# Performance work log

Measured on AMD Instinct MI355X. Metric: run time of the kernel, lower is better.

## Reference

```python
import jax, jax.numpy as jnp
import numpy as np

N, D, H, E, K = 8192, 1024, 4096, 8, 2


def setup_inputs() -> dict:
    key = jax.random.key(0)
    ks = jax.random.split(key, 4)
    scaled = lambda k, shp, fan: (jax.random.normal(k, shp, jnp.float32) / np.sqrt(fan).astype(np.float32))
    return {
        "x": jax.random.normal(ks[0], (N, D), jnp.float32),
        "Wg": scaled(ks[1], (D, E), D),
        "bg": jnp.zeros((E,), jnp.float32),
        "W1": scaled(ks[2], (E, D, H), D),
        "b1": jnp.zeros((E, H), jnp.float32),
        "W2": scaled(ks[3], (E, H, D), H),
        "b2": jnp.zeros((E, D), jnp.float32),
    }


def reference(x, Wg, bg, W1, b1, W2, b2):
    # Gating: softmax over experts, top-k selection, renormalize top-k probs.
    gate_probs = jax.nn.softmax(x @ Wg + bg, axis=-1)            # [N, E]
    topk_p, topk_i = jax.lax.top_k(gate_probs, K)                # [N, K]
    topk_p = topk_p / topk_p.sum(axis=-1, keepdims=True)
    onehot = jax.nn.one_hot(topk_i, E, dtype=x.dtype)            # [N, K, E]
    # Per-token combine weight for each expert (0 if expert not in top-k).
    w = (onehot * topk_p[..., None]).sum(axis=1)                 # [N, E]

    out = jnp.zeros_like(x)
    for e in range(E):  # fixed small loop over structurally distinct experts
        h = jax.nn.relu(x @ W1[e] + b1[e])                       # dropout = identity (eval)
        out = out + w[:, e:e + 1] * (h @ W2[e] + b2[e])

    # Load-balancing auxiliary loss.
    importance = gate_probs.sum(axis=0)
    importance = importance / importance.sum()
    load = onehot.sum(axis=(0, 1)) / (x.shape[0] * K)            # [E]
    lb_loss = E * (importance * load).sum()
    return out, lb_loss
```

## Files before the change

### kernel.cpp

```cpp
#include <hip/hip_runtime.h>
#include <hip/hip_bf16.h>
#include <math.h>

#define NTOK 8192
#define DDIM 1024
#define HDIM 4096
#define NEXP 8
#define KTOP 2
#define MAXROWS 17408
#define MAXTILES 136

typedef __bf16 bf16x8 __attribute__((ext_vector_type(8)));
typedef float f32x4 __attribute__((ext_vector_type(4)));

#define GAS __attribute__((address_space(1)))
#define LAS __attribute__((address_space(3)))

__device__ __forceinline__ void async16(const void* g, void* l) {
  __builtin_amdgcn_global_load_lds((GAS void*)g, (LAS void*)l, 16, 0, 0);
}

#define XB_OFF     ((size_t)0)
#define W1T_OFF    (XB_OFF + (size_t)NTOK*DDIM*2)
#define W2T_OFF    (W1T_OFF + (size_t)NEXP*DDIM*HDIM*2)
#define HB_OFF     (W2T_OFF + (size_t)NEXP*HDIM*DDIM*2)
#define ROWTOK_OFF (HB_OFF + (size_t)MAXROWS*HDIM*2)
#define ROWW_OFF   (ROWTOK_OFF + (size_t)MAXROWS*4)
#define TOKE_OFF   (ROWW_OFF + (size_t)MAXROWS*4)
#define TOKW_OFF   (TOKE_OFF + (size_t)NTOK*KTOP*4)
#define TILEE_OFF  (TOKW_OFF + (size_t)NTOK*KTOP*4)
#define CNT_OFF    (TILEE_OFF + (size_t)256*4)
#define POS_OFF    (CNT_OFF + 64)
#define IMP_OFF    (POS_OFF + 64)
#define META_OFF   (IMP_OFF + 64)

__global__ void init_kernel(int* counts, float* importance) {
  if (threadIdx.x < NEXP) { counts[threadIdx.x] = 0; importance[threadIdx.x] = 0.f; }
}

__global__ void zero_out_kernel(float* __restrict__ out) {
  size_t i = ((size_t)blockIdx.x * blockDim.x + threadIdx.x) * 4;
  if (i < (size_t)NTOK * DDIM) {
    *(float4*)(out + i) = make_float4(0.f, 0.f, 0.f, 0.f);
  }
}

__global__ void cast_x_kernel(const float* __restrict__ src, __hip_bfloat16* __restrict__ dst) {
  size_t i = ((size_t)blockIdx.x * blockDim.x + threadIdx.x) * 4;
  if (i < (size_t)NTOK * DDIM) {
    float4 v = *(const float4*)(src + i);
    dst[i + 0] = __float2bfloat16(v.x);
    dst[i + 1] = __float2bfloat16(v.y);
    dst[i + 2] = __float2bfloat16(v.z);
    dst[i + 3] = __float2bfloat16(v.w);
  }
}

__global__ __launch_bounds__(256) void transpose_cast_kernel(
    const float* __restrict__ src, __hip_bfloat16* __restrict__ dst, int R, int C) {
  __shared__ float tile[64][65];
  const int e = blockIdx.z;
  const float* s = src + (size_t)e * R * C;
  __hip_bfloat16* d = dst + (size_t)e * R * C;
  const int c0 = blockIdx.x * 64, r0 = blockIdx.y * 64;
  const int tx = threadIdx.x & 63, ty = threadIdx.x >> 6;
#pragma unroll
  for (int i = ty; i < 64; i += 4)
    tile[i][tx] = s[(size_t)(r0 + i) * C + c0 + tx];
  __syncthreads();
#pragma unroll
  for (int i = ty; i < 64; i += 4)
    d[(size_t)(c0 + i) * R + r0 + tx] = __float2bfloat16(tile[tx][i]);
}

__global__ __launch_bounds__(256) void gating_kernel(
    const float* __restrict__ x, const float* __restrict__ Wg, const float* __restrict__ bg,
    int* __restrict__ tok_e, float* __restrict__ tok_w,
    int* __restrict__ counts, float* __restrict__ importance) {
  const int tid = threadIdx.x, wid = tid >> 6, lane = tid & 63;
  const int t = blockIdx.x * 32 + wid * 8 + (lane >> 3);
  const int e = lane & 7;
  const float* xr = x + (size_t)t * DDIM;
  double dot = 0.0;
  for (int d = 0; d < DDIM; d += 4) {
    float4 xv = *(const float4*)(xr + d);
    dot += (double)xv.x * (double)Wg[(d + 0) * NEXP + e];
    dot += (double)xv.y * (double)Wg[(d + 1) * NEXP + e];
    dot += (double)xv.z * (double)Wg[(d + 2) * NEXP + e];
    dot += (double)xv.w * (double)Wg[(d + 3) * NEXP + e];
  }
  double logit = dot + (double)bg[e];
  double m = logit;
  for (int off = 1; off < 8; off <<= 1) {
    double o = __shfl_xor(m, off, 64);
    m = o > m ? o : m;
  }
  double p = exp(logit - m);
  double s = p;
  for (int off = 1; off < 8; off <<= 1) s += __shfl_xor(s, off, 64);
  float prob = (float)(p / s);

  __shared__ float imp[NEXP];
  __shared__ int cnt[NEXP];
  if (tid < NEXP) { imp[tid] = 0.f; cnt[tid] = 0; }
  __syncthreads();
  atomicAdd(&imp[e], prob);

  float bp = prob; int be = e;
  for (int off = 1; off < 8; off <<= 1) {
    float op = __shfl_xor(bp, off, 64); int oe = __shfl_xor(be, off, 64);
    if (op > bp || (op == bp && oe < be)) { bp = op; be = oe; }
  }
  float p2 = (e == be) ? -1.f : prob;
  float sp = p2; int se = e;
  for (int off = 1; off < 8; off <<= 1) {
    float op = __shfl_xor(sp, off, 64); int oe = __shfl_xor(se, off, 64);
    if (op > sp || (op == sp && oe < se)) { sp = op; se = oe; }
  }
  if (e == 0) {
    float tsum = bp + sp;
    tok_e[t * 2 + 0] = be; tok_e[t * 2 + 1] = se;
    tok_w[t * 2 + 0] = bp / tsum; tok_w[t * 2 + 1] = sp / tsum;
    atomicAdd(&cnt[be], 1); atomicAdd(&cnt[se], 1);
  }
  __syncthreads();
  if (tid < NEXP) {
    atomicAdd(&counts[tid], cnt[tid]);
    atomicAdd(&importance[tid], imp[tid]);
  }
}

__global__ void offsets_kernel(const int* __restrict__ counts, int* pos, int* tile_expert,
                               int* meta, int* row_token) {
  if (threadIdx.x == 0) {
    int pb = 0, tb = 0;
    for (int e = 0; e < NEXP; e++) {
      pos[e] = pb;
      int tiles = (counts[e] + 127) >> 7;
      for (int tt = 0; tt < tiles; ++tt) tile_expert[tb + tt] = e;
      pb += tiles * 128; tb += tiles;
    }
    meta[0] = tb;
  }
  __syncthreads();
  for (int i = threadIdx.x; i < MAXROWS; i += blockDim.x) row_token[i] = -1;
}

__global__ void scatter_kernel(const int* __restrict__ tok_e, const float* __restrict__ tok_w,
                               int* __restrict__ pos, int* __restrict__ row_token,
                               float* __restrict__ row_weight) {
  __shared__ int lcnt[NEXP], lbase[NEXP];
  const int t = blockIdx.x * 256 + threadIdx.x;
  if (threadIdx.x < NEXP) lcnt[threadIdx.x] = 0;
  __syncthreads();
  const int e0 = tok_e[t * 2 + 0], e1 = tok_e[t * 2 + 1];
  const int s0 = atomicAdd(&lcnt[e0], 1);
  const int s1 = atomicAdd(&lcnt[e1], 1);
  __syncthreads();
  if (threadIdx.x < NEXP) lbase[threadIdx.x] = atomicAdd(&pos[threadIdx.x], lcnt[threadIdx.x]);
  __syncthreads();
  int r0 = lbase[e0] + s0; row_token[r0] = t; row_weight[r0] = tok_w[t * 2 + 0];
  int r1 = lbase[e1] + s1; row_token[r1] = t; row_weight[r1] = tok_w[t * 2 + 1];
}

__global__ __launch_bounds__(256) void gemm1_kernel(
    const __hip_bfloat16* __restrict__ xb, const __hip_bfloat16* __restrict__ w1t,
    const float* __restrict__ b1, __hip_bfloat16* __restrict__ hb,
    const int* __restrict__ row_token, const int* __restrict__ tile_expert,
    const int* __restrict__ meta) {
  const int tile_y = blockIdx.y;
  if (tile_y >= meta[0]) return;
  const int n0 = blockIdx.x * 128;
  const int e = tile_expert[tile_y];
  const int r0 = tile_y * 128;
  const int tid = threadIdx.x;
  const int wid = tid >> 6, lane = tid & 63;

  __shared__ __align__(16) __hip_bfloat16 As[128 * 32];
  __shared__ __align__(16) __hip_bfloat16 Bs[128 * 32];

  const int srow = wid * 32 + (lane >> 2);
  const int scol = (lane & 3) * 8;
  int t0 = row_token[r0 + srow];      if (t0 < 0) t0 = 0;
  int t1 = row_token[r0 + srow + 16]; if (t1 < 0) t1 = 0;
  const __hip_bfloat16* ga0 = xb + (size_t)t0 * DDIM + scol;
  const __hip_bfloat16* ga1 = xb + (size_t)t1 * DDIM + scol;
  const __hip_bfloat16* gb0 = w1t + ((size_t)e * HDIM + n0 + srow) * DDIM + scol;
  const __hip_bfloat16* gb1 = gb0 + (size_t)16 * DDIM;
  __hip_bfloat16* lA0 = &As[(wid * 32 + 0) * 32];
  __hip_bfloat16* lA1 = &As[(wid * 32 + 16) * 32];
  __hip_bfloat16* lB0 = &Bs[(wid * 32 + 0) * 32];
  __hip_bfloat16* lB1 = &Bs[(wid * 32 + 16) * 32];

  f32x4 acc[4][4] = {};
  const int wm = (wid & 1) * 64, wn = (wid >> 1) * 64;
  const int fr = lane & 15;
  const int kq = (lane >> 4) * 8;

  for (int kt = 0; kt < DDIM / 32; ++kt) {
    __syncthreads();
    async16(ga0, lA0); async16(ga1, lA1);
    async16(gb0, lB0); async16(gb1, lB1);
    ga0 += 32; ga1 += 32; gb0 += 32; gb1 += 32;
    __syncthreads();
    bf16x8 av[4], bv[4];
#pragma unroll
    for (int i = 0; i < 4; i++) av[i] = *(const bf16x8*)&As[(wm + i * 16 + fr) * 32 + kq];
#pragma unroll
    for (int j = 0; j < 4; j++) bv[j] = *(const bf16x8*)&Bs[(wn + j * 16 + fr) * 32 + kq];
#pragma unroll
    for (int i = 0; i < 4; i++)
#pragma unroll
      for (int j = 0; j < 4; j++)
        acc[i][j] = __builtin_amdgcn_mfma_f32_16x16x32_bf16(av[i], bv[j], acc[i][j], 0, 0, 0);
  }

  const int crow = (lane >> 4) * 4;
  const int ccol = lane & 15;
#pragma unroll
  for (int j = 0; j < 4; j++) {
    const int gc = n0 + wn + j * 16 + ccol;
    const float bias = b1[e * HDIM + gc];
#pragma unroll
    for (int i = 0; i < 4; i++) {
      const int grb = r0 + wm + i * 16 + crow;
#pragma unroll
      for (int r = 0; r < 4; r++) {
        float v = acc[i][j][r] + bias;
        v = v > 0.f ? v : 0.f;
        hb[(size_t)(grb + r) * HDIM + gc] = __float2bfloat16(v);
      }
    }
  }
}

__global__ __launch_bounds__(256) void gemm2_kernel(
    const __hip_bfloat16* __restrict__ hb, const __hip_bfloat16* __restrict__ w2t,
    const float* __restrict__ b2, float* __restrict__ out,
    const int* __restrict__ row_token, const float* __restrict__ row_weight,
    const int* __restrict__ tile_expert, const int* __restrict__ meta) {
  const int tile_y = blockIdx.y;
  if (tile_y >= meta[0]) return;
  const int n0 = blockIdx.x * 128;
  const int e = tile_expert[tile_y];
  const int r0 = tile_y * 128;
  const int tid = threadIdx.x;
  const int wid = tid >> 6, lane = tid & 63;

  __shared__ __align__(16) __hip_bfloat16 As[128 * 32];
  __shared__ __align__(16) __hip_bfloat16 Bs[128 * 32];

  const int srow = wid * 32 + (lane >> 2);
  const int scol = (lane & 3) * 8;
  const __hip_bfloat16* ga0 = hb + (size_t)(r0 + srow) * HDIM + scol;
  const __hip_bfloat16* ga1 = ga0 + (size_t)16 * HDIM;
  const __hip_bfloat16* gb0 = w2t + ((size_t)e * DDIM + n0 + srow) * HDIM + scol;
  const __hip_bfloat16* gb1 = gb0 + (size_t)16 * HDIM;
  __hip_bfloat16* lA0 = &As[(wid * 32 + 0) * 32];
  __hip_bfloat16* lA1 = &As[(wid * 32 + 16) * 32];
  __hip_bfloat16* lB0 = &Bs[(wid * 32 + 0) * 32];
  __hip_bfloat16* lB1 = &Bs[(wid * 32 + 16) * 32];

  f32x4 acc[4][4] = {};
  const int wm = (wid & 1) * 64, wn = (wid >> 1) * 64;
  const int fr = lane & 15;
  const int kq = (lane >> 4) * 8;

  for (int kt = 0; kt < HDIM / 32; ++kt) {
    __syncthreads();
    async16(ga0, lA0); async16(ga1, lA1);
    async16(gb0, lB0); async16(gb1, lB1);
    ga0 += 32; ga1 += 32; gb0 += 32; gb1 += 32;
    __syncthreads();
    bf16x8 av[4], bv[4];
#pragma unroll
    for (int i = 0; i < 4; i++) av[i] = *(const bf16x8*)&As[(wm + i * 16 + fr) * 32 + kq];
#pragma unroll
    for (int j = 0; j < 4; j++) bv[j] = *(const bf16x8*)&Bs[(wn + j * 16 + fr) * 32 + kq];
#pragma unroll
    for (int i = 0; i < 4; i++)
#pragma unroll
      for (int j = 0; j < 4; j++)
        acc[i][j] = __builtin_amdgcn_mfma_f32_16x16x32_bf16(av[i], bv[j], acc[i][j], 0, 0, 0);
  }

  const int crow = (lane >> 4) * 4;
  const int ccol = lane & 15;
#pragma unroll
  for (int i = 0; i < 4; i++) {
#pragma unroll
    for (int r = 0; r < 4; r++) {
      const int rr = r0 + wm + i * 16 + crow + r;
      const int tok = row_token[rr];
      if (tok < 0) continue;
      const float w = row_weight[rr];
#pragma unroll
      for (int j = 0; j < 4; j++) {
        const int gc = n0 + wn + j * 16 + ccol;
        float v = w * (acc[i][j][r] + b2[e * DDIM + gc]);
        atomicAdd(out + (size_t)tok * DDIM + gc, v);
      }
    }
  }
}

__global__ void finalize_kernel(const float* __restrict__ importance,
                                const int* __restrict__ counts, float* __restrict__ lb_out) {
  if (threadIdx.x == 0 && blockIdx.x == 0) {
    float s = 0.f;
    for (int e = 0; e < NEXP; e++) s += importance[e];
    float lb = 0.f;
    for (int e = 0; e < NEXP; e++)
      lb += (importance[e] / s) * ((float)counts[e] / (float)(NTOK * KTOP));
    lb_out[0] = (float)NEXP * lb;
  }
}

extern "C" void kernel_launch(void* const* d_in, const int* in_sizes, int n_in,
                              void* d_out, int out_size, void* d_ws, size_t ws_size,
                              hipStream_t stream) {
  (void)in_sizes; (void)n_in; (void)out_size; (void)ws_size;
  const float* x  = (const float*)d_in[0];
  const float* Wg = (const float*)d_in[1];
  const float* bg = (const float*)d_in[2];
  const float* W1 = (const float*)d_in[3];
  const float* b1 = (const float*)d_in[4];
  const float* W2 = (const float*)d_in[5];
  const float* b2 = (const float*)d_in[6];
  float* out = (float*)d_out;

  char* ws = (char*)d_ws;
  __hip_bfloat16* xb  = (__hip_bfloat16*)(ws + XB_OFF);
  __hip_bfloat16* w1t = (__hip_bfloat16*)(ws + W1T_OFF);
  __hip_bfloat16* w2t = (__hip_bfloat16*)(ws + W2T_OFF);
  __hip_bfloat16* hb  = (__hip_bfloat16*)(ws + HB_OFF);
  int*   row_token  = (int*)(ws + ROWTOK_OFF);
  float* row_weight = (float*)(ws + ROWW_OFF);
  int*   tok_e  = (int*)(ws + TOKE_OFF);
  float* tok_w  = (float*)(ws + TOKW_OFF);
  int*   tile_e = (int*)(ws + TILEE_OFF);
  int*   counts = (int*)(ws + CNT_OFF);
  int*   pos    = (int*)(ws + POS_OFF);
  float* importance = (float*)(ws + IMP_OFF);
  int*   meta   = (int*)(ws + META_OFF);

  init_kernel<<<1, 64, 0, stream>>>(counts, importance);
  zero_out_kernel<<<NTOK * DDIM / 4 / 256, 256, 0, stream>>>(out);
  cast_x_kernel<<<NTOK * DDIM / 4 / 256, 256, 0, stream>>>(x, xb);
  transpose_cast_kernel<<<dim3(HDIM / 64, DDIM / 64, NEXP), 256, 0, stream>>>(W1, w1t, DDIM, HDIM);
  transpose_cast_kernel<<<dim3(DDIM / 64, HDIM / 64, NEXP), 256, 0, stream>>>(W2, w2t, HDIM, DDIM);
  gating_kernel<<<NTOK / 32, 256, 0, stream>>>(x, Wg, bg, tok_e, tok_w, counts, importance);
  offsets_kernel<<<1, 256, 0, stream>>>(counts, pos, tile_e, meta, row_token);
  scatter_kernel<<<NTOK / 256, 256, 0, stream>>>(tok_e, tok_w, pos, row_token, row_weight);
  gemm1_kernel<<<dim3(HDIM / 128, MAXTILES), 256, 0, stream>>>(xb, w1t, b1, hb, row_token, tile_e, meta);
  gemm2_kernel<<<dim3(DDIM / 128, MAXTILES), 256, 0, stream>>>(hb, w2t, b2, out, row_token, row_weight, tile_e, meta);
  finalize_kernel<<<1, 64, 0, stream>>>(importance, counts, out + (size_t)NTOK * DDIM);
}
```

Baseline: 888.4 us.

## Deepen GEMM K-tile with XOR-swizzled LDS and replace atomic scatter with combine pass

Both expert GEMMs now stage 64-wide K tiles in LDS using an XOR swizzle, which halves the barrier count per K and avoids LDS bank conflicts. GEMM2 no longer does fp32 atomicAdd into the output. It writes per-row bf16 results into a buffer that reuses the W1 transpose space, and a new combine kernel gathers the two rows per token, weights them, and writes the output, so the zero-fill kernel is removed. The transpose-cast kernel uses float4 loads and 8-byte stores. The combine path adds bf16 rounding of expert outputs before weighting and one extra pass over memory.

```diff
diff --git a/kernel.cpp b/kernel.cpp
--- a/kernel.cpp
+++ b/kernel.cpp
@@ -22,13 +22,15 @@
 
 #define XB_OFF     ((size_t)0)
 #define W1T_OFF    (XB_OFF + (size_t)NTOK*DDIM*2)
+#define ROWOUT_OFF W1T_OFF
 #define W2T_OFF    (W1T_OFF + (size_t)NEXP*DDIM*HDIM*2)
 #define HB_OFF     (W2T_OFF + (size_t)NEXP*HDIM*DDIM*2)
 #define ROWTOK_OFF (HB_OFF + (size_t)MAXROWS*HDIM*2)
 #define ROWW_OFF   (ROWTOK_OFF + (size_t)MAXROWS*4)
 #define TOKE_OFF   (ROWW_OFF + (size_t)MAXROWS*4)
 #define TOKW_OFF   (TOKE_OFF + (size_t)NTOK*KTOP*4)
-#define TILEE_OFF  (TOKW_OFF + (size_t)NTOK*KTOP*4)
+#define TOKROW_OFF (TOKW_OFF + (size_t)NTOK*KTOP*4)
+#define TILEE_OFF  (TOKROW_OFF + (size_t)NTOK*KTOP*4)
 #define CNT_OFF    (TILEE_OFF + (size_t)256*4)
 #define POS_OFF    (CNT_OFF + 64)
 #define IMP_OFF    (POS_OFF + 64)
@@ -36,13 +38,6 @@
 
 __global__ void init_kernel(int* counts, float* importance) {
   if (threadIdx.x < NEXP) { counts[threadIdx.x] = 0; importance[threadIdx.x] = 0.f; }
-}
-
-__global__ void zero_out_kernel(float* __restrict__ out) {
-  size_t i = ((size_t)blockIdx.x * blockDim.x + threadIdx.x) * 4;
-  if (i < (size_t)NTOK * DDIM) {
-    *(float4*)(out + i) = make_float4(0.f, 0.f, 0.f, 0.f);
-  }
 }
 
 __global__ void cast_x_kernel(const float* __restrict__ src, __hip_bfloat16* __restrict__ dst) {
@@ -63,14 +58,29 @@
   const float* s = src + (size_t)e * R * C;
   __hip_bfloat16* d = dst + (size_t)e * R * C;
   const int c0 = blockIdx.x * 64, r0 = blockIdx.y * 64;
-  const int tx = threadIdx.x & 63, ty = threadIdx.x >> 6;
-#pragma unroll
-  for (int i = ty; i < 64; i += 4)
-    tile[i][tx] = s[(size_t)(r0 + i) * C + c0 + tx];
-  __syncthreads();
-#pragma unroll
-  for (int i = ty; i < 64; i += 4)
-    d[(size_t)(c0 + i) * R + r0 + tx] = __float2bfloat16(tile[tx][i]);
+  const int tc = (threadIdx.x & 15) * 4;
+  const int tr = threadIdx.x >> 4;
+#pragma unroll
+  for (int p = 0; p < 4; ++p) {
+    float4 v = *(const float4*)&s[(size_t)(r0 + tr + p * 16) * C + c0 + tc];
+    tile[tr + p * 16][tc + 0] = v.x;
+    tile[tr + p * 16][tc + 1] = v.y;
+    tile[tr + p * 16][tc + 2] = v.z;
+    tile[tr + p * 16][tc + 3] = v.w;
+  }
+  __syncthreads();
+  const int oc = threadIdx.x >> 4;
+  const int orr = (threadIdx.x & 15) * 4;
+#pragma unroll
+  for (int p = 0; p < 4; ++p) {
+    const int c = oc + p * 16;
+    __hip_bfloat16 tmp[4];
+    tmp[0] = __float2bfloat16(tile[orr + 0][c]);
+    tmp[1] = __float2bfloat16(tile[orr + 1][c]);
+    tmp[2] = __float2bfloat16(tile[orr + 2][c]);
+    tmp[3] = __float2bfloat16(tile[orr + 3][c]);
+    *(ushort4*)&d[(size_t)(c0 + c) * R + r0 + orr] = *(ushort4*)tmp;
+  }
 }
 
 __global__ __launch_bounds__(256) void gating_kernel(
@@ -148,7 +158,7 @@
 
 __global__ void scatter_kernel(const int* __restrict__ tok_e, const float* __restrict__ tok_w,
                                int* __restrict__ pos, int* __restrict__ row_token,
-                               float* __restrict__ row_weight) {
+                               float* __restrict__ row_weight, int* __restrict__ tok_row) {
   __shared__ int lcnt[NEXP], lbase[NEXP];
   const int t = blockIdx.x * 256 + threadIdx.x;
   if (threadIdx.x < NEXP) lcnt[threadIdx.x] = 0;
@@ -159,8 +169,8 @@
   __syncthreads();
   if (threadIdx.x < NEXP) lbase[threadIdx.x] = atomicAdd(&pos[threadIdx.x], lcnt[threadIdx.x]);
   __syncthreads();
-  int r0 = lbase[e0] + s0; row_token[r0] = t; row_weight[r0] = tok_w[t * 2 + 0];
-  int r1 = lbase[e1] + s1; row_token[r1] = t; row_weight[r1] = tok_w[t * 2 + 1];
+  int r0 = lbase[e0] + s0; row_token[r0] = t; row_weight[r0] = tok_w[t * 2 + 0]; tok_row[t * 2 + 0] = r0;
+  int r1 = lbase[e1] + s1; row_token[r1] = t; row_weight[r1] = tok_w[t * 2 + 1]; tok_row[t * 2 + 1] = r1;
 }
 
 __global__ __launch_bounds__(256) void gemm1_kernel(
@@ -176,43 +186,51 @@
   const int tid = threadIdx.x;
   const int wid = tid >> 6, lane = tid & 63;
 
-  __shared__ __align__(16) __hip_bfloat16 As[128 * 32];
-  __shared__ __align__(16) __hip_bfloat16 Bs[128 * 32];
-
-  const int srow = wid * 32 + (lane >> 2);
-  const int scol = (lane & 3) * 8;
-  int t0 = row_token[r0 + srow];      if (t0 < 0) t0 = 0;
-  int t1 = row_token[r0 + srow + 16]; if (t1 < 0) t1 = 0;
-  const __hip_bfloat16* ga0 = xb + (size_t)t0 * DDIM + scol;
-  const __hip_bfloat16* ga1 = xb + (size_t)t1 * DDIM + scol;
-  const __hip_bfloat16* gb0 = w1t + ((size_t)e * HDIM + n0 + srow) * DDIM + scol;
-  const __hip_bfloat16* gb1 = gb0 + (size_t)16 * DDIM;
-  __hip_bfloat16* lA0 = &As[(wid * 32 + 0) * 32];
-  __hip_bfloat16* lA1 = &As[(wid * 32 + 16) * 32];
-  __hip_bfloat16* lB0 = &Bs[(wid * 32 + 0) * 32];
-  __hip_bfloat16* lB1 = &Bs[(wid * 32 + 16) * 32];
+  __shared__ __align__(16) __hip_bfloat16 As[128 * 64];
+  __shared__ __align__(16) __hip_bfloat16 Bs[128 * 64];
+
+  const int lrow = lane >> 3;
+  const int g = ((lane & 7) ^ lrow) * 8;
+  const __hip_bfloat16* ga[4]; const __hip_bfloat16* gb[4];
+  __hip_bfloat16 *lA[4], *lB[4];
+#pragma unroll
+  for (int c = 0; c < 4; ++c) {
+    const int srow = wid * 32 + c * 8 + lrow;
+    int t = row_token[r0 + srow]; if (t < 0) t = 0;
+    ga[c] = xb + (size_t)t * DDIM + g;
+    gb[c] = w1t + ((size_t)e * HDIM + n0 + srow) * DDIM + g;
+    lA[c] = &As[(wid * 32 + c * 8) * 64];
+    lB[c] = &Bs[(wid * 32 + c * 8) * 64];
+  }
 
   f32x4 acc[4][4] = {};
   const int wm = (wid & 1) * 64, wn = (wid >> 1) * 64;
   const int fr = lane & 15;
-  const int kq = (lane >> 4) * 8;
-
-  for (int kt = 0; kt < DDIM / 32; ++kt) {
+  const int swz0 = ((0 + (lane >> 4)) ^ (lane & 7)) * 8;
+  const int swz1 = ((4 + (lane >> 4)) ^ (lane & 7)) * 8;
+
+  for (int kt = 0; kt < DDIM / 64; ++kt) {
     __syncthreads();
-    async16(ga0, lA0); async16(ga1, lA1);
-    async16(gb0, lB0); async16(gb1, lB1);
-    ga0 += 32; ga1 += 32; gb0 += 32; gb1 += 32;
+#pragma unroll
+    for (int c = 0; c < 4; ++c) {
+      async16(ga[c], lA[c]); async16(gb[c], lB[c]);
+      ga[c] += 64; gb[c] += 64;
+    }
     __syncthreads();
-    bf16x8 av[4], bv[4];
-#pragma unroll
-    for (int i = 0; i < 4; i++) av[i] = *(const bf16x8*)&As[(wm + i * 16 + fr) * 32 + kq];
-#pragma unroll
-    for (int j = 0; j < 4; j++) bv[j] = *(const bf16x8*)&Bs[(wn + j * 16 + fr) * 32 + kq];
-#pragma unroll
-    for (int i = 0; i < 4; i++)
-#pragma unroll
-      for (int j = 0; j < 4; j++)
-        acc[i][j] = __builtin_amdgcn_mfma_f32_16x16x32_bf16(av[i], bv[j], acc[i][j], 0, 0, 0);
+#pragma unroll
+    for (int ks = 0; ks < 2; ++ks) {
+      const int off = ks ? swz1 : swz0;
+      bf16x8 av[4], bv[4];
+#pragma unroll
+      for (int i = 0; i < 4; i++) av[i] = *(const bf16x8*)&As[(wm + i * 16 + fr) * 64 + off];
+#pragma unroll
+      for (int j = 0; j < 4; j++) bv[j] = *(const bf16x8*)&Bs[(wn + j * 16 + fr) * 64 + off];
+#pragma unroll
+      for (int i = 0; i < 4; i++)
+#pragma unroll
+        for (int j = 0; j < 4; j++)
+          acc[i][j] = __builtin_amdgcn_mfma_f32_16x16x32_bf16(av[i], bv[j], acc[i][j], 0, 0, 0);
+    }
   }
 
   const int crow = (lane >> 4) * 4;
@@ -236,8 +254,7 @@
 
 __global__ __launch_bounds__(256) void gemm2_kernel(
     const __hip_bfloat16* __restrict__ hb, const __hip_bfloat16* __restrict__ w2t,
-    const float* __restrict__ b2, float* __restrict__ out,
-    const int* __restrict__ row_token, const float* __restrict__ row_weight,
+    const float* __restrict__ b2, __hip_bfloat16* __restrict__ rowout,
     const int* __restrict__ tile_expert, const int* __restrict__ meta) {
   const int tile_y = blockIdx.y;
   if (tile_y >= meta[0]) return;
@@ -247,61 +264,84 @@
   const int tid = threadIdx.x;
   const int wid = tid >> 6, lane = tid & 63;
 
-  __shared__ __align__(16) __hip_bfloat16 As[128 * 32];
-  __shared__ __align__(16) __hip_bfloat16 Bs[128 * 32];
-
-  const int srow = wid * 32 + (lane >> 2);
-  const int scol = (lane & 3) * 8;
-  const __hip_bfloat16* ga0 = hb + (size_t)(r0 + srow) * HDIM + scol;
-  const __hip_bfloat16* ga1 = ga0 + (size_t)16 * HDIM;
-  const __hip_bfloat16* gb0 = w2t + ((size_t)e * DDIM + n0 + srow) * HDIM + scol;
-  const __hip_bfloat16* gb1 = gb0 + (size_t)16 * HDIM;
-  __hip_bfloat16* lA0 = &As[(wid * 32 + 0) * 32];
-  __hip_bfloat16* lA1 = &As[(wid * 32 + 16) * 32];
-  __hip_bfloat16* lB0 = &Bs[(wid * 32 + 0) * 32];
-  __hip_bfloat16* lB1 = &Bs[(wid * 32 + 16) * 32];
+  __shared__ __align__(16) __hip_bfloat16 As[128 * 64];
+  __shared__ __align__(16) __hip_bfloat16 Bs[128 * 64];
+
+  const int lrow = lane >> 3;
+  const int g = ((lane & 7) ^ lrow) * 8;
+  const __hip_bfloat16* ga[4]; const __hip_bfloat16* gb[4];
+  __hip_bfloat16 *lA[4], *lB[4];
+#pragma unroll
+  for (int c = 0; c < 4; ++c) {
+    const int srow = wid * 32 + c * 8 + lrow;
+    ga[c] = hb + ((size_t)r0 + srow) * HDIM + g;
+    gb[c] = w2t + ((size_t)e * DDIM + n0 + srow) * HDIM + g;
+    lA[c] = &As[(wid * 32 + c * 8) * 64];
+    lB[c] = &Bs[(wid * 32 + c * 8) * 64];
+  }
 
   f32x4 acc[4][4] = {};
   const int wm = (wid & 1) * 64, wn = (wid >> 1) * 64;
   const int fr = lane & 15;
-  const int kq = (lane >> 4) * 8;
-
-  for (int kt = 0; kt < HDIM / 32; ++kt) {
+  const int swz0 = ((0 + (lane >> 4)) ^ (lane & 7)) * 8;
+  const int swz1 = ((4 + (lane >> 4)) ^ (lane & 7)) * 8;
+
+  for (int kt = 0; kt < HDIM / 64; ++kt) {
     __syncthreads();
-    async16(ga0, lA0); async16(ga1, lA1);
-    async16(gb0, lB0); async16(gb1, lB1);
-    ga0 += 32; ga1 += 32; gb0 += 32; gb1 += 32;
+#pragma unroll
+    for (int c = 0; c < 4; ++c) {
+      async16(ga[c], lA[c]); async16(gb[c], lB[c]);
+      ga[c] += 64; gb[c] += 64;
+    }
     __syncthreads();
-    bf16x8 av[4], bv[4];
-#pragma unroll
-    for (int i = 0; i < 4; i++) av[i] = *(const bf16x8*)&As[(wm + i * 16 + fr) * 32 + kq];
-#pragma unroll
-    for (int j = 0; j < 4; j++) bv[j] = *(const bf16x8*)&Bs[(wn + j * 16 + fr) * 32 + kq];
-#pragma unroll
-    for (int i = 0; i < 4; i++)
-#pragma unroll
-      for (int j = 0; j < 4; j++)
-        acc[i][j] = __builtin_amdgcn_mfma_f32_16x16x32_bf16(av[i], bv[j], acc[i][j], 0, 0, 0);
+#pragma unroll
+    for (int ks = 0; ks < 2; ++ks) {
+      const int off = ks ? swz1 : swz0;
+      bf16x8 av[4], bv[4];
+#pragma unroll
+      for (int i = 0; i < 4; i++) av[i] = *(const bf16x8*)&As[(wm + i * 16 + fr) * 64 + off];
+#pragma unroll
+      for (int j = 0; j < 4; j++) bv[j] = *(const bf16x8*)&Bs[(wn + j * 16 + fr) * 64 + off];
+#pragma unroll
+      for (int i = 0; i < 4; i++)
+#pragma unroll
+        for (int j = 0; j < 4; j++)
+          acc[i][j] = __builtin_amdgcn_mfma_f32_16x16x32_bf16(av[i], bv[j], acc[i][j], 0, 0, 0);
+    }
   }
 
   const int crow = (lane >> 4) * 4;
   const int ccol = lane & 15;
 #pragma unroll
-  for (int i = 0; i < 4; i++) {
-#pragma unroll
-    for (int r = 0; r < 4; r++) {
-      const int rr = r0 + wm + i * 16 + crow + r;
-      const int tok = row_token[rr];
-      if (tok < 0) continue;
-      const float w = row_weight[rr];
-#pragma unroll
-      for (int j = 0; j < 4; j++) {
-        const int gc = n0 + wn + j * 16 + ccol;
-        float v = w * (acc[i][j][r] + b2[e * DDIM + gc]);
-        atomicAdd(out + (size_t)tok * DDIM + gc, v);
-      }
-    }
-  }
+  for (int j = 0; j < 4; j++) {
+    const int gc = n0 + wn + j * 16 + ccol;
+    const float bias = b2[e * DDIM + gc];
+#pragma unroll
+    for (int i = 0; i < 4; i++) {
+      const int rr = r0 + wm + i * 16 + crow;
+#pragma unroll
+      for (int r = 0; r < 4; r++)
+        rowout[(size_t)(rr + r) * DDIM + gc] = __float2bfloat16(acc[i][j][r] + bias);
+    }
+  }
+}
+
+__global__ __launch_bounds__(256) void combine_kernel(
+    const __hip_bfloat16* __restrict__ rowout, const int* __restrict__ tok_row,
+    const float* __restrict__ row_weight, float* __restrict__ out) {
+  const int idx = blockIdx.x * 256 + threadIdx.x;
+  const int t = idx >> 7;
+  const int d = (idx & 127) * 8;
+  const int r0 = tok_row[t * 2 + 0], r1 = tok_row[t * 2 + 1];
+  const float w0 = row_weight[r0], w1 = row_weight[r1];
+  bf16x8 a = *(const bf16x8*)&rowout[(size_t)r0 * DDIM + d];
+  bf16x8 b = *(const bf16x8*)&rowout[(size_t)r1 * DDIM + d];
+  float o[8];
+#pragma unroll
+  for (int k = 0; k < 8; k++) o[k] = w0 * (float)a[k] + w1 * (float)b[k];
+  float* dst = out + (size_t)t * DDIM + d;
+  *(float4*)(dst + 0) = make_float4(o[0], o[1], o[2], o[3]);
+  *(float4*)(dst + 4) = make_float4(o[4], o[5], o[6], o[7]);
 }
 
 __global__ void finalize_kernel(const float* __restrict__ importance,
@@ -330,29 +370,31 @@
   float* out = (float*)d_out;
 
   char* ws = (char*)d_ws;
-  __hip_bfloat16* xb  = (__hip_bfloat16*)(ws + XB_OFF);
-  __hip_bfloat16* w1t = (__hip_bfloat16*)(ws + W1T_OFF);
-  __hip_bfloat16* w2t = (__hip_bfloat16*)(ws + W2T_OFF);
-  __hip_bfloat16* hb  = (__hip_bfloat16*)(ws + HB_OFF);
+  __hip_bfloat16* xb     = (__hip_bfloat16*)(ws + XB_OFF);
+  __hip_bfloat16* w1t    = (__hip_bfloat16*)(ws + W1T_OFF);
+  __hip_bfloat16* rowout = (__hip_bfloat16*)(ws + ROWOUT_OFF);
+  __hip_bfloat16* w2t    = (__hip_bfloat16*)(ws + W2T_OFF);
+  __hip_bfloat16* hb     = (__hip_bfloat16*)(ws + HB_OFF);
   int*   row_token  = (int*)(ws + ROWTOK_OFF);
   float* row_weight = (float*)(ws + ROWW_OFF);
-  int*   tok_e  = (int*)(ws + TOKE_OFF);
-  float* tok_w  = (float*)(ws + TOKW_OFF);
-  int*   tile_e = (int*)(ws + TILEE_OFF);
-  int*   counts = (int*)(ws + CNT_OFF);
-  int*   pos    = (int*)(ws + POS_OFF);
+  int*   tok_e   = (int*)(ws + TOKE_OFF);
+  float* tok_w   = (float*)(ws + TOKW_OFF);
+  int*   tok_row = (int*)(ws + TOKROW_OFF);
+  int*   tile_e  = (int*)(ws + TILEE_OFF);
+  int*   counts  = (int*)(ws + CNT_OFF);
+  int*   pos     = (int*)(ws + POS_OFF);
   float* importance = (float*)(ws + IMP_OFF);
-  int*   meta   = (int*)(ws + META_OFF);
+  int*   meta    = (int*)(ws + META_OFF);
 
   init_kernel<<<1, 64, 0, stream>>>(counts, importance);
-  zero_out_kernel<<<NTOK * DDIM / 4 / 256, 256, 0, stream>>>(out);
   cast_x_kernel<<<NTOK * DDIM / 4 / 256, 256, 0, stream>>>(x, xb);
   transpose_cast_kernel<<<dim3(HDIM / 64, DDIM / 64, NEXP), 256, 0, stream>>>(W1, w1t, DDIM, HDIM);
   transpose_cast_kernel<<<dim3(DDIM / 64, HDIM / 64, NEXP), 256, 0, stream>>>(W2, w2t, HDIM, DDIM);
   gating_kernel<<<NTOK / 32, 256, 0, stream>>>(x, Wg, bg, tok_e, tok_w, counts, importance);
   offsets_kernel<<<1, 256, 0, stream>>>(counts, pos, tile_e, meta, row_token);
-  scatter_kernel<<<NTOK / 256, 256, 0, stream>>>(tok_e, tok_w, pos, row_token, row_weight);
+  scatter_kernel<<<NTOK / 256, 256, 0, stream>>>(tok_e, tok_w, pos, row_token, row_weight, tok_row);
   gemm1_kernel<<<dim3(HDIM / 128, MAXTILES), 256, 0, stream>>>(xb, w1t, b1, hb, row_token, tile_e, meta);
-  gemm2_kernel<<<dim3(DDIM / 128, MAXTILES), 256, 0, stream>>>(hb, w2t, b2, out, row_token, row_weight, tile_e, meta);
+  gemm2_kernel<<<dim3(DDIM / 128, MAXTILES), 256, 0, stream>>>(hb, w2t, b2, rowout, tile_e, meta);
+  combine_kernel<<<NTOK * 128 / 256, 256, 0, stream>>>(rowout, tok_row, row_weight, out);
   finalize_kernel<<<1, 64, 0, stream>>>(importance, counts, out + (size_t)NTOK * DDIM);
 }
```

Measured after the change: 861.4 us. 3.0% less time.
